# Kernel optimization log

Measured on AMD Instinct MI355X. Metric: run time of the kernel, lower is better.

Reference implementation:

```python
import jax, jax.numpy as jnp
import numpy as np

B, N, K, C, NH = 2, 16384, 16, 256, 4
HD = C // NH  # head_dim = 64


def knn_gather(feat, idx):
    # feat: [B, N, D], idx: [B, N, K] -> [B, N, K, D]
    b, n, k = idx.shape
    d = feat.shape[-1]
    flat = jnp.take_along_axis(feat, idx.reshape(b, n * k)[..., None], axis=1)
    return flat.reshape(b, n, k, d)


def setup_inputs() -> dict:
    key = jax.random.key(0)
    ks = jax.random.split(key, 16)
    s_c = 1.0 / np.sqrt(C)
    s_4 = 1.0 / np.sqrt(4.0)
    s_hd = 1.0 / np.sqrt(HD)
    return {
        'h': jax.random.normal(ks[0], (B, N, C), jnp.float32),
        'P': jax.random.normal(ks[1], (B, 3, N), jnp.float32),
        'idx': jax.random.randint(ks[2], (B, N, K), 0, N),
        'Wq': jax.random.normal(ks[3], (C, C), jnp.float32) * s_c,
        'Wk': jax.random.normal(ks[4], (C, C), jnp.float32) * s_c,
        'Wv': jax.random.normal(ks[5], (C, C), jnp.float32) * s_c,
        'Wp1': jax.random.normal(ks[6], (4, C), jnp.float32) * s_4,
        'bp1': jnp.zeros((C,), jnp.float32),
        'Wp2': jax.random.normal(ks[7], (C, C), jnp.float32) * s_c,
        'bp2': jnp.zeros((C,), jnp.float32),
        'Wa1': jax.random.normal(ks[8], (HD, HD), jnp.float32) * s_hd,
        'ba1': jnp.zeros((HD,), jnp.float32),
        'Wa2': jax.random.normal(ks[9], (HD, 1), jnp.float32) * s_hd,
        'ba2': jnp.zeros((1,), jnp.float32),
        'Wo': jax.random.normal(ks[10], (C, C), jnp.float32) * s_c,
        'bo': jnp.zeros((C,), jnp.float32),
    }


def reference(h, P, idx, Wq, Wk, Wv, Wp1, bp1, Wp2, bp2, Wa1, ba1, Wa2, ba2, Wo, bo):
    b, n, c = h.shape
    P_t = jnp.swapaxes(P, 1, 2)                       # [B, N, 3]
    P_nbr = knn_gather(P_t, idx)                      # [B, N, K, 3]
    rel_pos = P_nbr - P_t[:, :, None, :]              # [B, N, K, 3]
    dist = jnp.linalg.norm(rel_pos, axis=-1, keepdims=True)
    geom = jnp.concatenate([rel_pos, dist], axis=-1)  # [B, N, K, 4]
    pe = jax.nn.relu(geom @ Wp1 + bp1) @ Wp2 + bp2    # [B, N, K, C]
    pe = pe.reshape(b, n, K, NH, HD)

    Q = (h @ Wq).reshape(b, n, 1, NH, HD)
    K_nbr = knn_gather(h @ Wk, idx).reshape(b, n, K, NH, HD)
    V_nbr = knn_gather(h @ Wv, idx).reshape(b, n, K, NH, HD)

    relation = Q - K_nbr + pe                          # [B, N, K, NH, HD]
    logits = jax.nn.relu(relation @ Wa1 + ba1) @ Wa2 + ba2  # [B, N, K, NH, 1]
    attn = jax.nn.softmax(logits, axis=2)              # softmax over K
    agg = jnp.sum(attn * (V_nbr + pe), axis=2)         # [B, N, NH, HD]
    agg = agg.reshape(b, n, c)
    return agg @ Wo + bo
```

## Files before the change

### kernel.cpp

```cpp
#include <hip/hip_runtime.h>
#include <hip/hip_bf16.h>

#define BB 2
#define NN 16384
#define KK 16
#define CC 256
#define NHH 4
#define HDD 64
#define BN (BB*NN)

typedef __attribute__((ext_vector_type(8))) short short8;
typedef __attribute__((ext_vector_type(4))) float f32x4;

__device__ __forceinline__ float bf2f(unsigned short u) {
    union { unsigned u32; float f; } x; x.u32 = ((unsigned)u) << 16; return x.f;
}
__device__ __forceinline__ unsigned short f2bf(float f) {
    union { float f; unsigned u; } x; x.f = f;
    unsigned r = x.u + 0x7FFFu + ((x.u >> 16) & 1u);
    return (unsigned short)(r >> 16);
}

__global__ __launch_bounds__(256) void prep_kernel(
    const float* __restrict__ Wq, const float* __restrict__ Wk,
    const float* __restrict__ Wv, const float* __restrict__ Wp2,
    const float* __restrict__ Wo, const float* __restrict__ Wa1,
    const float* __restrict__ bp2, const float* __restrict__ ba1,
    unsigned short* WqaT, unsigned short* WkaT, unsigned short* WvT,
    unsigned short* WpeaT, unsigned short* Wp2T, unsigned short* WoT,
    float* b_u)
{
    const int z = blockIdx.y;
    const int t = threadIdx.x;
    if (z < 3) {
        const float* W = (z == 0) ? Wq : (z == 1) ? Wk : Wp2;
        unsigned short* out = (z == 0) ? WqaT : (z == 1) ? WkaT : WpeaT;
        const int k = blockIdx.x;
        __shared__ float wrow[CC];
        __shared__ float a1[HDD * HDD];
        wrow[t] = W[k * CC + t];
        for (int i = t; i < HDD * HDD; i += 256) a1[i] = Wa1[i];
        __syncthreads();
        const int c = t;
        const int h0 = c & ~63;
        const int cl = c & 63;
        float s = 0.f;
        #pragma unroll 8
        for (int j = 0; j < HDD; ++j) s += wrow[h0 + j] * a1[j * HDD + cl];
        out[c * CC + k] = f2bf(s);
    } else if (z < 6) {
        const float* W = (z == 3) ? Wv : (z == 4) ? Wp2 : Wo;
        unsigned short* out = (z == 3) ? WvT : (z == 4) ? Wp2T : WoT;
        const int k = blockIdx.x;
        out[t * CC + k] = f2bf(W[k * CC + t]);
    } else {
        if (blockIdx.x != 0) return;
        __shared__ float a1[HDD * HDD];
        for (int i = t; i < HDD * HDD; i += 256) a1[i] = Wa1[i];
        __syncthreads();
        const int c = t;
        const int h0 = c & ~63;
        const int cl = c & 63;
        float s = ba1[cl];
        #pragma unroll 8
        for (int j = 0; j < HDD; ++j) s += bp2[h0 + j] * a1[j * HDD + cl];
        b_u[c] = s;
    }
}

__global__ __launch_bounds__(256) void h2bf_kernel(const float* __restrict__ h,
                                                   unsigned short* __restrict__ hbf)
{
    const int i = blockIdx.x * blockDim.x + threadIdx.x;
    const float4 v = ((const float4*)h)[i];
    ushort4 o;
    o.x = f2bf(v.x); o.y = f2bf(v.y); o.z = f2bf(v.z); o.w = f2bf(v.w);
    ((ushort4*)hbf)[i] = o;
}

template<bool FINAL>
__global__ __launch_bounds__(256) void gemm64_kernel(
    const unsigned short* __restrict__ A,
    const unsigned short* __restrict__ BT0, const unsigned short* __restrict__ BT1,
    const unsigned short* __restrict__ BT2,
    unsigned short* D0, unsigned short* D1, unsigned short* D2,
    float* Dout, const float* __restrict__ bias)
{
    const int m0 = blockIdx.x * 64;
    const unsigned short* BT;
    unsigned short* Dst = nullptr;
    if (!FINAL) {
        const int z = blockIdx.y;
        BT  = (z == 0) ? BT0 : (z == 1) ? BT1 : BT2;
        Dst = (z == 0) ? D0  : (z == 1) ? D1  : D2;
    } else {
        BT = BT0;
    }

    __shared__ __align__(16) unsigned short As[64 * 264];
    const int t = threadIdx.x;
    #pragma unroll
    for (int i = 0; i < 8; ++i) {
        const int flat = i * 2048 + t * 8;
        const int r = flat >> 8, c = flat & 255;
        short8 v = *(const short8*)(A + (size_t)(m0 + r) * CC + c);
        *(short8*)(&As[r * 264 + c]) = v;
    }
    __syncthreads();

    const int lane = t & 63, w = t >> 6;
    const int lr = lane & 15, lg = lane >> 4;

    f32x4 acc[4][4];
    #pragma unroll
    for (int mi = 0; mi < 4; ++mi)
        #pragma unroll
        for (int ni = 0; ni < 4; ++ni) acc[mi][ni] = (f32x4){0.f, 0.f, 0.f, 0.f};

    #pragma unroll
    for (int kk = 0; kk < 8; ++kk) {
        const int ko = kk * 32 + lg * 8;
        short8 a[4];
        #pragma unroll
        for (int mi = 0; mi < 4; ++mi)
            a[mi] = *(const short8*)(&As[(mi * 16 + lr) * 264 + ko]);
        #pragma unroll
        for (int ni = 0; ni < 4; ++ni) {
            const int col = w * 64 + ni * 16 + lr;
            short8 b = *(const short8*)(BT + (size_t)col * CC + ko);
            #pragma unroll
            for (int mi = 0; mi < 4; ++mi)
                acc[mi][ni] = __builtin_amdgcn_mfma_f32_16x16x32_bf16(a[mi], b, acc[mi][ni], 0, 0, 0);
        }
    }

    #pragma unroll
    for (int mi = 0; mi < 4; ++mi) {
        #pragma unroll
        for (int ni = 0; ni < 4; ++ni) {
            const int col = w * 64 + ni * 16 + lr;
            #pragma unroll
            for (int reg = 0; reg < 4; ++reg) {
                const int row = m0 + mi * 16 + lg * 4 + reg;
                const float v = acc[mi][ni][reg];
                if (FINAL) Dout[(size_t)row * CC + col] = v + bias[col];
                else       Dst[(size_t)row * CC + col] = f2bf(v);
            }
        }
    }
}

__global__ __launch_bounds__(256, 3) void fused_attn_kernel(
    const float* __restrict__ P, const int* __restrict__ idx,
    const float* __restrict__ Wp1, const float* __restrict__ bp1,
    const float* __restrict__ Wa2, const float* __restrict__ bp2,
    const unsigned short* __restrict__ QAbf, const unsigned short* __restrict__ KAbf,
    const unsigned short* __restrict__ Vbf,  const unsigned short* __restrict__ WpeaT,
    const unsigned short* __restrict__ Wp2T, const float* __restrict__ b_u,
    unsigned short* __restrict__ aggbf)
{
    const int pt0 = blockIdx.x * 4;
    const int b = pt0 >> 14;
    const int n0 = pt0 & (NN - 1);
    const int t = threadIdx.x;

    __shared__ int nbrL[64];
    __shared__ __align__(16) float geomL[64][4];
    __shared__ __align__(16) unsigned short QAsb[4 * CC];
    __shared__ float buL[CC];
    __shared__ float wa2L[HDD];
    __shared__ __align__(16) unsigned short hidL[64 * 264];
    __shared__ float logitsL[64][NHH];
    __shared__ float attnL[64][NHH];
    __shared__ __align__(16) unsigned short hbarL[16 * 264];
    __shared__ unsigned short vbarL[16 * 72];

    if (t < 64) {
        const int g = t >> 4, k = t & 15;
        const int nb = idx[(size_t)(pt0 + g) * KK + k];
        nbrL[t] = nb;
        const float* Pb = P + (size_t)b * 3 * NN;
        const int nc = n0 + g;
        const float rx = Pb[nb] - Pb[nc];
        const float ry = Pb[NN + nb] - Pb[NN + nc];
        const float rz = Pb[2 * NN + nb] - Pb[2 * NN + nc];
        const float d = sqrtf(rx * rx + ry * ry + rz * rz);
        geomL[t][0] = rx; geomL[t][1] = ry; geomL[t][2] = rz; geomL[t][3] = d;
    }
    {
        const int e = t * 4;
        *(ushort4*)(&QAsb[e]) = *(const ushort4*)(QAbf + (size_t)pt0 * CC + e);
    }
    buL[t] = b_u[t];
    if (t < 64) wa2L[t] = Wa2[t];
    __syncthreads();

    {
        const int c = t;
        const float w0 = Wp1[c], w1 = Wp1[CC + c], w2 = Wp1[2 * CC + c], w3 = Wp1[3 * CC + c];
        const float bb = bp1[c];
        #pragma unroll 4
        for (int r = 0; r < 64; ++r) {
            const float4 gm = *(const float4*)(&geomL[r][0]);
            float v = fmaf(gm.x, w0, fmaf(gm.y, w1, fmaf(gm.z, w2, fmaf(gm.w, w3, bb))));
            hidL[r * 264 + c] = f2bf(fmaxf(v, 0.f));
        }
    }
    __syncthreads();

    const int lane = t & 63, w = t >> 6;
    const int lr = lane & 15, lg = lane >> 4;

    f32x4 acc[4][4];
    #pragma unroll
    for (int mi = 0; mi < 4; ++mi)
        #pragma unroll
        for (int ni = 0; ni < 4; ++ni) acc[mi][ni] = (f32x4){0.f, 0.f, 0.f, 0.f};

    #pragma unroll
    for (int kk = 0; kk < 8; ++kk) {
        const int ko = kk * 32 + lg * 8;
        short8 a[4];
        #pragma unroll
        for (int mi = 0; mi < 4; ++mi)
            a[mi] = *(const short8*)(&hidL[(mi * 16 + lr) * 264 + ko]);
        #pragma unroll
        for (int ni = 0; ni < 4; ++ni) {
            const int col = w * 64 + ni * 16 + lr;
            short8 bfr = *(const short8*)(WpeaT + (size_t)col * CC + ko);
            #pragma unroll
            for (int mi = 0; mi < 4; ++mi)
                acc[mi][ni] = __builtin_amdgcn_mfma_f32_16x16x32_bf16(a[mi], bfr, acc[mi][ni], 0, 0, 0);
        }
    }

    #pragma unroll
    for (int mi = 0; mi < 4; ++mi) {
        unsigned short ka[4][4];
        #pragma unroll
        for (int reg = 0; reg < 4; ++reg) {
            const int r = mi * 16 + lg * 4 + reg;
            const size_t base = ((size_t)b * NN + nbrL[r]) * CC;
            #pragma unroll
            for (int ni = 0; ni < 4; ++ni)
                ka[reg][ni] = KAbf[base + w * 64 + ni * 16 + lr];
        }
        #pragma unroll
        for (int reg = 0; reg < 4; ++reg) {
            float pl = 0.f;
            #pragma unroll
            for (int ni = 0; ni < 4; ++ni) {
                const int c = w * 64 + ni * 16 + lr;
                const float u = bf2f(QAsb[mi * CC + c]) - bf2f(ka[reg][ni])
                              + acc[mi][ni][reg] + buL[c];
                pl += fmaxf(u, 0.f) * wa2L[ni * 16 + lr];
            }
            pl += __shfl_xor(pl, 1);
            pl += __shfl_xor(pl, 2);
            pl += __shfl_xor(pl, 4);
            pl += __shfl_xor(pl, 8);
            if (lr == 0) logitsL[mi * 16 + lg * 4 + reg][w] = pl;
        }
    }
    __syncthreads();

    {
        const int p = t >> 4, k = t & 15;
        const int g = p >> 2, hh = p & 3;
        const float v = logitsL[g * 16 + k][hh];
        float m = v;
        m = fmaxf(m, __shfl_xor(m, 1));
        m = fmaxf(m, __shfl_xor(m, 2));
        m = fmaxf(m, __shfl_xor(m, 4));
        m = fmaxf(m, __shfl_xor(m, 8));
        const float e = __expf(v - m);
        float s = e;
        s += __shfl_xor(s, 1);
        s += __shfl_xor(s, 2);
        s += __shfl_xor(s, 4);
        s += __shfl_xor(s, 8);
        attnL[g * 16 + k][hh] = e / s;
    }
    __syncthreads();

    {
        const int c = t;
        #pragma unroll
        for (int g = 0; g < 4; ++g) {
            float hv[16];
            #pragma unroll
            for (int k = 0; k < 16; ++k) hv[k] = bf2f(hidL[(g * 16 + k) * 264 + c]);
            #pragma unroll
            for (int hh = 0; hh < NHH; ++hh) {
                float s = 0.f;
                #pragma unroll
                for (int k = 0; k < 16; ++k) s += attnL[g * 16 + k][hh] * hv[k];
                hbarL[(g * 4 + hh) * 264 + c] = f2bf(s);
            }
        }
    }
    {
        const int d = lane;
        #pragma unroll
        for (int i = 0; i < 4; ++i) {
            const int gh = w * 4 + i;
            const int g = gh >> 2, hh = gh & 3;
            float s = 0.f;
            #pragma unroll
            for (int k = 0; k < 16; ++k) {
                const int r = g * 16 + k;
                const size_t src = ((size_t)b * NN + nbrL[r]) * CC + hh * 64 + d;
                s += attnL[r][hh] * bf2f(Vbf[src]);
            }
            vbarL[gh * 72 + d] = f2bf(s);
        }
    }
    __syncthreads();

    f32x4 acc2[4];
    #pragma unroll
    for (int ni = 0; ni < 4; ++ni) acc2[ni] = (f32x4){0.f, 0.f, 0.f, 0.f};
    #pragma unroll
    for (int kk = 0; kk < 8; ++kk) {
        const int ko = kk * 32 + lg * 8;
        short8 a = *(const short8*)(&hbarL[lr * 264 + ko]);
        #pragma unroll
        for (int ni = 0; ni < 4; ++ni) {
            const int col = w * 64 + ni * 16 + lr;
            short8 bfr = *(const short8*)(Wp2T + (size_t)col * CC + ko);
            acc2[ni] = __builtin_amdgcn_mfma_f32_16x16x32_bf16(a, bfr, acc2[ni], 0, 0, 0);
        }
    }
    #pragma unroll
    for (int ni = 0; ni < 4; ++ni) {
        const int cl = ni * 16 + lr;
        const int c = w * 64 + cl;
        float pv;
        if      (w == 0) pv = acc2[ni][0];
        else if (w == 1) pv = acc2[ni][1];
        else if (w == 2) pv = acc2[ni][2];
        else             pv = acc2[ni][3];
        const float v = pv + bf2f(vbarL[(lg * 4 + w) * 72 + cl]) + bp2[c];
        aggbf[(size_t)(pt0 + lg) * CC + c] = f2bf(v);
    }
}

extern "C" void kernel_launch(void* const* d_in, const int* in_sizes, int n_in,
                              void* d_out, int out_size, void* d_ws, size_t ws_size,
                              hipStream_t stream)
{
    const float* h   = (const float*)d_in[0];
    const float* P   = (const float*)d_in[1];
    const int*   idx = (const int*)d_in[2];
    const float* Wq  = (const float*)d_in[3];
    const float* Wk  = (const float*)d_in[4];
    const float* Wv  = (const float*)d_in[5];
    const float* Wp1 = (const float*)d_in[6];
    const float* bp1 = (const float*)d_in[7];
    const float* Wp2 = (const float*)d_in[8];
    const float* bp2 = (const float*)d_in[9];
    const float* Wa1 = (const float*)d_in[10];
    const float* ba1 = (const float*)d_in[11];
    const float* Wa2 = (const float*)d_in[12];
    const float* Wo  = (const float*)d_in[14];
    const float* bo  = (const float*)d_in[15];

    char* ws = (char*)d_ws;
    const size_t MB16 = 16777216;
    unsigned short* WqaT  = (unsigned short*)(ws + 0);
    unsigned short* WkaT  = (unsigned short*)(ws + 131072);
    unsigned short* WvT   = (unsigned short*)(ws + 262144);
    unsigned short* WpeaT = (unsigned short*)(ws + 393216);
    unsigned short* Wp2T  = (unsigned short*)(ws + 524288);
    unsigned short* WoT   = (unsigned short*)(ws + 655360);
    float*          b_u   = (float*)(ws + 786432);
    const size_t base = 1 << 20;
    unsigned short* hbf   = (unsigned short*)(ws + base + 0 * MB16);
    unsigned short* QAbf  = (unsigned short*)(ws + base + 1 * MB16);
    unsigned short* KAbf  = (unsigned short*)(ws + base + 2 * MB16);
    unsigned short* Vbf   = (unsigned short*)(ws + base + 3 * MB16);
    unsigned short* aggbf = (unsigned short*)(ws + base + 4 * MB16);
    if (ws_size < base + 5 * MB16) return;

    prep_kernel<<<dim3(256, 7), 256, 0, stream>>>(Wq, Wk, Wv, Wp2, Wo, Wa1, bp2, ba1,
                                                  WqaT, WkaT, WvT, WpeaT, Wp2T, WoT, b_u);
    h2bf_kernel<<<BN * CC / 4 / 256, 256, 0, stream>>>(h, hbf);
    gemm64_kernel<false><<<dim3(BN / 64, 3), 256, 0, stream>>>(
        hbf, WqaT, WkaT, WvT, QAbf, KAbf, Vbf, nullptr, nullptr);
    fused_attn_kernel<<<BN / 4, 256, 0, stream>>>(P, idx, Wp1, bp1, Wa2, bp2,
                                                  QAbf, KAbf, Vbf, WpeaT, Wp2T, b_u, aggbf);
    gemm64_kernel<true><<<dim3(BN / 64, 1), 256, 0, stream>>>(
        aggbf, WoT, nullptr, nullptr, nullptr, nullptr, nullptr, (float*)d_out, bo);
}
```

Before: 413.8 us.

## Fuse softmax into logit pass, shrink LDS, raise occupancy to four blocks

The Q/bias terms move out of shared memory and into registers, and they seed the MFMA accumulator so they no longer have to be added per element. The softmax over neighbours is now done inside the logit wavefront using lane shuffles, which removes the logits buffer and one block barrier. The hbar buffer now reuses the hidL region, and launch bounds go from 3 to 4 blocks per CU so more waves can hide gather latency. The cost is more register pressure under the tighter occupancy target, which could cause spills, plus redundant global loads of QA per thread.

```diff
diff --git a/kernel.cpp b/kernel.cpp
--- a/kernel.cpp
+++ b/kernel.cpp
@@ -150,7 +150,7 @@
     }
 }
 
-__global__ __launch_bounds__(256, 3) void fused_attn_kernel(
+__global__ __launch_bounds__(256, 4) void fused_attn_kernel(
     const float* __restrict__ P, const int* __restrict__ idx,
     const float* __restrict__ Wp1, const float* __restrict__ bp1,
     const float* __restrict__ Wa2, const float* __restrict__ bp2,
@@ -163,17 +163,26 @@
     const int b = pt0 >> 14;
     const int n0 = pt0 & (NN - 1);
     const int t = threadIdx.x;
+    const int lane = t & 63, w = t >> 6;
+    const int lr = lane & 15, lg = lane >> 4;
 
     __shared__ int nbrL[64];
     __shared__ __align__(16) float geomL[64][4];
-    __shared__ __align__(16) unsigned short QAsb[4 * CC];
-    __shared__ float buL[CC];
-    __shared__ float wa2L[HDD];
     __shared__ __align__(16) unsigned short hidL[64 * 264];
-    __shared__ float logitsL[64][NHH];
     __shared__ float attnL[64][NHH];
-    __shared__ __align__(16) unsigned short hbarL[16 * 264];
     __shared__ unsigned short vbarL[16 * 72];
+
+    float qab[4][4];
+    float wa2v[4];
+    #pragma unroll
+    for (int ni = 0; ni < 4; ++ni) {
+        const int c = w * 64 + ni * 16 + lr;
+        wa2v[ni] = Wa2[ni * 16 + lr];
+        const float bu = b_u[c];
+        #pragma unroll
+        for (int mi = 0; mi < 4; ++mi)
+            qab[mi][ni] = bf2f(QAbf[(size_t)(pt0 + mi) * CC + c]) + bu;
+    }
 
     if (t < 64) {
         const int g = t >> 4, k = t & 15;
@@ -187,12 +196,6 @@
         const float d = sqrtf(rx * rx + ry * ry + rz * rz);
         geomL[t][0] = rx; geomL[t][1] = ry; geomL[t][2] = rz; geomL[t][3] = d;
     }
-    {
-        const int e = t * 4;
-        *(ushort4*)(&QAsb[e]) = *(const ushort4*)(QAbf + (size_t)pt0 * CC + e);
-    }
-    buL[t] = b_u[t];
-    if (t < 64) wa2L[t] = Wa2[t];
     __syncthreads();
 
     {
@@ -208,14 +211,14 @@
     }
     __syncthreads();
 
-    const int lane = t & 63, w = t >> 6;
-    const int lr = lane & 15, lg = lane >> 4;
-
     f32x4 acc[4][4];
     #pragma unroll
     for (int mi = 0; mi < 4; ++mi)
         #pragma unroll
-        for (int ni = 0; ni < 4; ++ni) acc[mi][ni] = (f32x4){0.f, 0.f, 0.f, 0.f};
+        for (int ni = 0; ni < 4; ++ni) {
+            const float v = qab[mi][ni];
+            acc[mi][ni] = (f32x4){v, v, v, v};
+        }
 
     #pragma unroll
     for (int kk = 0; kk < 8; ++kk) {
@@ -245,41 +248,35 @@
             for (int ni = 0; ni < 4; ++ni)
                 ka[reg][ni] = KAbf[base + w * 64 + ni * 16 + lr];
         }
+        float pl[4];
         #pragma unroll
         for (int reg = 0; reg < 4; ++reg) {
-            float pl = 0.f;
+            float s = 0.f;
             #pragma unroll
             for (int ni = 0; ni < 4; ++ni) {
-                const int c = w * 64 + ni * 16 + lr;
-                const float u = bf2f(QAsb[mi * CC + c]) - bf2f(ka[reg][ni])
-                              + acc[mi][ni][reg] + buL[c];
-                pl += fmaxf(u, 0.f) * wa2L[ni * 16 + lr];
+                const float u = acc[mi][ni][reg] - bf2f(ka[reg][ni]);
+                s += fmaxf(u, 0.f) * wa2v[ni];
             }
-            pl += __shfl_xor(pl, 1);
-            pl += __shfl_xor(pl, 2);
-            pl += __shfl_xor(pl, 4);
-            pl += __shfl_xor(pl, 8);
-            if (lr == 0) logitsL[mi * 16 + lg * 4 + reg][w] = pl;
-        }
-    }
-    __syncthreads();
-
-    {
-        const int p = t >> 4, k = t & 15;
-        const int g = p >> 2, hh = p & 3;
-        const float v = logitsL[g * 16 + k][hh];
-        float m = v;
-        m = fmaxf(m, __shfl_xor(m, 1));
-        m = fmaxf(m, __shfl_xor(m, 2));
-        m = fmaxf(m, __shfl_xor(m, 4));
-        m = fmaxf(m, __shfl_xor(m, 8));
-        const float e = __expf(v - m);
-        float s = e;
-        s += __shfl_xor(s, 1);
-        s += __shfl_xor(s, 2);
-        s += __shfl_xor(s, 4);
-        s += __shfl_xor(s, 8);
-        attnL[g * 16 + k][hh] = e / s;
+            s += __shfl_xor(s, 1);
+            s += __shfl_xor(s, 2);
+            s += __shfl_xor(s, 4);
+            s += __shfl_xor(s, 8);
+            pl[reg] = s;
+        }
+        float m = fmaxf(fmaxf(pl[0], pl[1]), fmaxf(pl[2], pl[3]));
+        m = fmaxf(m, __shfl_xor(m, 16));
+        m = fmaxf(m, __shfl_xor(m, 32));
+        float e[4], s = 0.f;
+        #pragma unroll
+        for (int reg = 0; reg < 4; ++reg) { e[reg] = __expf(pl[reg] - m); s += e[reg]; }
+        s += __shfl_xor(s, 16);
+        s += __shfl_xor(s, 32);
+        const float inv = 1.f / s;
+        if (lr == 0) {
+            #pragma unroll
+            for (int reg = 0; reg < 4; ++reg)
+                attnL[mi * 16 + lg * 4 + reg][w] = e[reg] * inv;
+        }
     }
     __syncthreads();
 
@@ -295,7 +292,7 @@
                 float s = 0.f;
                 #pragma unroll
                 for (int k = 0; k < 16; ++k) s += attnL[g * 16 + k][hh] * hv[k];
-                hbarL[(g * 4 + hh) * 264 + c] = f2bf(s);
+                hidL[(g * 4 + hh) * 264 + c] = f2bf(s);
             }
         }
     }
@@ -323,7 +320,7 @@
     #pragma unroll
     for (int kk = 0; kk < 8; ++kk) {
         const int ko = kk * 32 + lg * 8;
-        short8 a = *(const short8*)(&hbarL[lr * 264 + ko]);
+        short8 a = *(const short8*)(&hidL[lr * 264 + ko]);
         #pragma unroll
         for (int ni = 0; ni < 4; ++ni) {
             const int col = w * 64 + ni * 16 + lr;
```

Result: slower. 515.7 us (+24.6%).
